# Optimization experiments

Measured on AMD Instinct MI355X. Metric: run time of the kernel, lower is better.

Reference implementation:

```python
import jax, jax.numpy as jnp
import numpy as np

D = 256      # hidden_size
H = 4        # num_attention_heads
DH = D // H  # dim per head = 64
L = 4        # num_hidden_layers
M = 266      # nb_features = int(64 * ln(64))
S = 4096     # seq len / max_position_embeddings
B = 4
LN_EPS = 1e-12


def layer_norm(x, g, b, eps=LN_EPS):
    mu = jnp.mean(x, -1, keepdims=True)
    var = jnp.var(x, -1, keepdims=True)
    return (x - mu) / jnp.sqrt(var + eps) * g + b


def softmax_kernel(x, proj, is_query, eps=1e-4):
    # x: [b,h,s,d], proj: [m,d] -> phi(x): [b,h,s,m] (FAVOR+ positive features)
    d = x.shape[-1]
    m = proj.shape[0]
    dn = d ** -0.25
    ratio = m ** -0.5
    dash = jnp.einsum('bhsd,md->bhsm', x, proj) * dn
    diag = jnp.sum(x * x, -1, keepdims=True) * 0.5 * (dn * dn)
    if is_query:
        stab = jnp.max(dash, -1, keepdims=True)  # per-query stabilizer
    else:
        stab = jnp.max(dash)  # global stabilizer for keys
    return ratio * (jnp.exp(dash - diag - stab) + eps)


def favor_attention(x, proj, Wq, bq, Wk, bk, Wv, bv, Wo, bo):
    b, s, d = x.shape
    split = lambda t: t.reshape(b, s, H, DH).transpose(0, 2, 1, 3)  # [b,h,s,dh]
    q = split(x @ Wq + bq)
    k = split(x @ Wk + bk)
    v = split(x @ Wv + bv)
    qp = softmax_kernel(q, proj, True)   # [b,h,s,m]
    kp = softmax_kernel(k, proj, False)  # [b,h,s,m]
    ksum = kp.sum(axis=2)                                  # [b,h,m]
    d_inv = 1.0 / jnp.einsum('bhsm,bhm->bhs', qp, ksum)    # normalizer
    ctx = jnp.einsum('bhsm,bhse->bhme', kp, v)             # [b,h,m,dh]
    out = jnp.einsum('bhsm,bhme,bhs->bhse', qp, ctx, d_inv)
    out = out.transpose(0, 2, 1, 3).reshape(b, s, d)
    return out @ Wo + bo


def _forward(input_embs, attention_mask, pos_emb, ln_g, ln_b, proj,
             Wq, bq, Wk, bk, Wv, bv, Wo, bo, ln1_g, ln1_b,
             W1, b1, W2, b2, ln2_g, ln2_b, p1_w, p1_b, p2_w, p2_b):
    b, s, d = input_embs.shape
    x = input_embs + pos_emb[:s][None]
    x = layer_norm(x, ln_g, ln_b)  # dropout is identity at eval
    for i in range(L):
        x = x + favor_attention(layer_norm(x, ln1_g[i], ln1_b[i]), proj[i],
                                Wq[i], bq[i], Wk[i], bk[i], Wv[i], bv[i], Wo[i], bo[i])
        h = layer_norm(x, ln2_g[i], ln2_b[i])
        x = x + (jax.nn.gelu(h @ W1[i] + b1[i]) @ W2[i] + b2[i])
    # AttentionPooling
    e = jnp.tanh(x @ p1_w + p1_b)
    alpha = jnp.exp(e @ p2_w + p2_b)            # [b,s,1]
    alpha = alpha * attention_mask[..., None]
    alpha = alpha / (jnp.sum(alpha, 1, keepdims=True) + 1e-8)
    return jnp.einsum('bsd,bs->bd', x, alpha[..., 0])


def setup_inputs() -> dict:
    key = jax.random.key(0)
    ks = iter(jax.random.split(key, 32))
    std = 0.02
    nrm = lambda shape: jax.random.normal(next(ks), shape, jnp.float32)
    return {
        'input_embs': nrm((B, S, D)),
        'attention_mask': jnp.ones((B, S), jnp.float32),
        'pos_emb': nrm((S, D)) * std,
        'ln_g': jnp.ones((D,), jnp.float32), 'ln_b': jnp.zeros((D,), jnp.float32),
        'proj': nrm((L, M, DH)),
        'Wq': nrm((L, D, D)) * std, 'bq': jnp.zeros((L, D), jnp.float32),
        'Wk': nrm((L, D, D)) * std, 'bk': jnp.zeros((L, D), jnp.float32),
        'Wv': nrm((L, D, D)) * std, 'bv': jnp.zeros((L, D), jnp.float32),
        'Wo': nrm((L, D, D)) * std, 'bo': jnp.zeros((L, D), jnp.float32),
        'ln1_g': jnp.ones((L, D), jnp.float32), 'ln1_b': jnp.zeros((L, D), jnp.float32),
        'W1': nrm((L, D, 4 * D)) * std, 'b1': jnp.zeros((L, 4 * D), jnp.float32),
        'W2': nrm((L, 4 * D, D)) * std, 'b2': jnp.zeros((L, D), jnp.float32),
        'ln2_g': jnp.ones((L, D), jnp.float32), 'ln2_b': jnp.zeros((L, D), jnp.float32),
        'p1_w': nrm((D, D)) * std, 'p1_b': jnp.zeros((D,), jnp.float32),
        'p2_w': nrm((D, 1)) * std, 'p2_b': jnp.zeros((1,), jnp.float32),
    }


def reference(input_embs, attention_mask, pos_emb, ln_g, ln_b, proj,
              Wq, bq, Wk, bk, Wv, bv, Wo, bo, ln1_g, ln1_b,
              W1, b1, W2, b2, ln2_g, ln2_b, p1_w, p1_b, p2_w, p2_b):
    return _forward(input_embs, attention_mask, pos_emb, ln_g, ln_b, proj,
                    Wq, bq, Wk, bk, Wv, bv, Wo, bo, ln1_g, ln1_b,
                    W1, b1, W2, b2, ln2_g, ln2_b, p1_w, p1_b, p2_w, p2_b)
```

## Files before the change

### kernel.cpp

```cpp
#include <hip/hip_runtime.h>
#include <math.h>


#define WS_ALIGN(x) (((x) + 255) & ~(size_t)255)

#define DN 0.35355339059327373f
#define DIAGC 0.0625f
#define RATIO 0.06131393394849658f
#define FEPS 1e-4f

typedef __attribute__((__ext_vector_type__(8))) __bf16 bf16x8;
typedef __attribute__((__ext_vector_type__(4))) float f32x4;

__device__ __forceinline__ float wredsum(float v) {
    v += __shfl_xor(v, 32); v += __shfl_xor(v, 16); v += __shfl_xor(v, 8);
    v += __shfl_xor(v, 4);  v += __shfl_xor(v, 2);  v += __shfl_xor(v, 1);
    return v;
}
__device__ __forceinline__ float wredmax(float v) {
    v = fmaxf(v, __shfl_xor(v, 32)); v = fmaxf(v, __shfl_xor(v, 16));
    v = fmaxf(v, __shfl_xor(v, 8));  v = fmaxf(v, __shfl_xor(v, 4));
    v = fmaxf(v, __shfl_xor(v, 2));  v = fmaxf(v, __shfl_xor(v, 1));
    return v;
}

__device__ __forceinline__ unsigned short f2bf(float f) {
    unsigned u = __builtin_bit_cast(unsigned, f);
    return (unsigned short)((u + 0x7fffu + ((u >> 16) & 1u)) >> 16);
}
__device__ __forceinline__ float blo(unsigned x) { return __builtin_bit_cast(float, x << 16); }
__device__ __forceinline__ float bhi(unsigned x) { return __builtin_bit_cast(float, x & 0xffff0000u); }
__device__ __forceinline__ float sumsq8(uint4 u) {
    float s = 0.f;
    s += blo(u.x)*blo(u.x) + bhi(u.x)*bhi(u.x);
    s += blo(u.y)*blo(u.y) + bhi(u.y)*bhi(u.y);
    s += blo(u.z)*blo(u.z) + bhi(u.z)*bhi(u.z);
    s += blo(u.w)*blo(u.w) + bhi(u.w)*bhi(u.w);
    return s;
}
__device__ __forceinline__ unsigned pack2(float a, float b) {
    return (unsigned)f2bf(a) | ((unsigned)f2bf(b) << 16);
}

__device__ __forceinline__ void gload_lds16(const unsigned short* g, unsigned short* lds) {
    __builtin_amdgcn_global_load_lds(
        (const __attribute__((address_space(1))) unsigned int*)g,
        (__attribute__((address_space(3))) unsigned int*)lds, 16, 0, 0);
}

__global__ __launch_bounds__(256) void add_ln2_kernel(
    const float* __restrict__ in, const float* __restrict__ pos,
    const float* __restrict__ g0, const float* __restrict__ b0,
    const float* __restrict__ g1, const float* __restrict__ b1,
    float* __restrict__ xout, unsigned short* __restrict__ hout)
{
    int row = blockIdx.x, t = threadIdx.x;
    __shared__ float sred[4];
    float v = in[(size_t)row * 256 + t] + pos[(size_t)(row & 4095) * 256 + t];
    float s = wredsum(v);
    if ((t & 63) == 0) sred[t >> 6] = s;
    __syncthreads();
    float mean = (sred[0] + sred[1] + sred[2] + sred[3]) * (1.0f / 256.0f);
    float d = v - mean;
    __syncthreads();
    float sq = wredsum(d * d);
    if ((t & 63) == 0) sred[t >> 6] = sq;
    __syncthreads();
    float var = (sred[0] + sred[1] + sred[2] + sred[3]) * (1.0f / 256.0f);
    float y1 = d * rsqrtf(var + 1e-12f) * g0[t] + b0[t];
    xout[(size_t)row * 256 + t] = y1;
    __syncthreads();
    float s1 = wredsum(y1);
    if ((t & 63) == 0) sred[t >> 6] = s1;
    __syncthreads();
    float mean1 = (sred[0] + sred[1] + sred[2] + sred[3]) * (1.0f / 256.0f);
    float d1 = y1 - mean1;
    __syncthreads();
    float sq1 = wredsum(d1 * d1);
    if ((t & 63) == 0) sred[t >> 6] = sq1;
    __syncthreads();
    float var1 = (sred[0] + sred[1] + sred[2] + sred[3]) * (1.0f / 256.0f);
    hout[(size_t)row * 256 + t] = f2bf(d1 * rsqrtf(var1 + 1e-12f) * g1[t] + b1[t]);
}

__global__ __launch_bounds__(256) void cast_transpose_kernel(
    const float* __restrict__ in, unsigned short* __restrict__ out, int R, int C)
{
    __shared__ float tile[32][33];
    size_t zo = (size_t)blockIdx.z * R * C;
    int c0 = blockIdx.x * 32, r0 = blockIdx.y * 32;
    int t = threadIdx.x, tc = t & 31, tr = t >> 5;
#pragma unroll
    for (int j = 0; j < 4; j++)
        tile[tr + j * 8][tc] = in[zo + (size_t)(r0 + tr + j * 8) * C + c0 + tc];
    __syncthreads();
#pragma unroll
    for (int j = 0; j < 4; j++) {
        int cc = tr + j * 8, rr = tc;
        out[zo + (size_t)(c0 + cc) * R + r0 + rr] = f2bf(tile[rr][cc]);
    }
}

__global__ __launch_bounds__(256) void cast_transpose4_kernel(
    const float* __restrict__ i0, const float* __restrict__ i1,
    const float* __restrict__ i2, const float* __restrict__ i3,
    unsigned short* __restrict__ o0, unsigned short* __restrict__ o1,
    unsigned short* __restrict__ o2, unsigned short* __restrict__ o3)
{
    __shared__ float tile[32][33];
    int z = blockIdx.z;
    int which = z >> 2, layer = z & 3;
    const float* in = (which == 0) ? i0 : (which == 1) ? i1 : (which == 2) ? i2 : i3;
    unsigned short* out = (which == 0) ? o0 : (which == 1) ? o1 : (which == 2) ? o2 : o3;
    size_t zo = (size_t)layer * 65536;
    int c0 = blockIdx.x * 32, r0 = blockIdx.y * 32;
    int t = threadIdx.x, tc = t & 31, tr = t >> 5;
#pragma unroll
    for (int j = 0; j < 4; j++)
        tile[tr + j * 8][tc] = in[zo + (size_t)(r0 + tr + j * 8) * 256 + c0 + tc];
    __syncthreads();
#pragma unroll
    for (int j = 0; j < 4; j++) {
        int cc = tr + j * 8, rr = tc;
        out[zo + (size_t)(c0 + cc) * 256 + r0 + rr] = f2bf(tile[rr][cc]);
    }
}

__global__ __launch_bounds__(256) void proj_cast_kernel(
    const float* __restrict__ proj, unsigned short* __restrict__ projbf)
{
    int idx = blockIdx.x * 256 + threadIdx.x;
    if (idx >= 10240) return;
    int li = idx / 2560; int rem = idx - li * 2560;
    int m = rem >> 3; int c = rem & 7;
    uint4 pk = {0, 0, 0, 0};
    if (m < 266) {
        const float* src = proj + ((size_t)li * 266 + m) * 64 + c * 8;
        float4 f0 = *(const float4*)(src);
        float4 f1 = *(const float4*)(src + 4);
        pk.x = pack2(f0.x, f0.y); pk.y = pack2(f0.z, f0.w);
        pk.z = pack2(f1.x, f1.y); pk.w = pack2(f1.z, f1.w);
    }
    *(uint4*)(projbf + (size_t)idx * 8) = pk;
}

__global__ __launch_bounds__(256) void ctx_cast_kernel(
    const float* __restrict__ ctxT, unsigned short* __restrict__ ctxbf)
{
    int idx = blockIdx.x * 256 + threadIdx.x;
    int row = idx / 36;
    int c = idx - row * 36;
    int m = c * 8;
    uint4 pk = {0, 0, 0, 0};
    if (m < 272) {
        const float* src = ctxT + (size_t)row * 272 + m;
        float4 f0 = *(const float4*)(src);
        float4 f1 = *(const float4*)(src + 4);
        pk.x = pack2(f0.x, f0.y); pk.y = pack2(f0.z, f0.w);
        pk.z = pack2(f1.x, f1.y); pk.w = pack2(f1.z, f1.w);
    }
    *(uint4*)(ctxbf + (size_t)row * 288 + c * 8) = pk;
}

__global__ __launch_bounds__(256) void qkv_kernel(
    const unsigned short* __restrict__ A,
    const unsigned short* __restrict__ Wqt, const unsigned short* __restrict__ Wkt,
    const unsigned short* __restrict__ Wvt,
    const float* __restrict__ bq, const float* __restrict__ bk, const float* __restrict__ bv,
    unsigned short* __restrict__ qbf, unsigned short* __restrict__ kbf,
    unsigned short* __restrict__ vT)
{
    __shared__ unsigned short As[2][4096];
    __shared__ unsigned short Bs[2][2048];
    const int K = 256;
    int t = threadIdx.x;
    int bm = blockIdx.y * 128, bn = blockIdx.x * 64;
    int grp = bn >> 8, lbn = bn & 255;
    const unsigned short* Bt = (grp == 0) ? Wqt : (grp == 1) ? Wkt : Wvt;
    const float* bias = (grp == 0) ? bq : (grp == 1) ? bk : bv;
    int w = t >> 6, l = t & 63, lm16 = l & 15, quad = l >> 4;
    int gc8 = ((l & 3) ^ ((l >> 3) & 3)) * 8;
    int rc8 = (quad ^ ((lm16 >> 1) & 3)) * 8;
    const unsigned short* pa0 = A + (size_t)(bm + w * 16 + (l >> 2)) * K + gc8;
    const unsigned short* pa1 = pa0 + (size_t)64 * K;
    const unsigned short* pb0 = Bt + (size_t)(lbn + w * 16 + (l >> 2)) * K + gc8;
    auto stage = [&](int buf, int k0) {
        gload_lds16(pa0 + k0, &As[buf][w * 512]);
        gload_lds16(pa1 + k0, &As[buf][w * 512 + 2048]);
        gload_lds16(pb0 + k0, &Bs[buf][w * 512]);
    };
    stage(0, 0);
    f32x4 acc[2][4] = {};
    __syncthreads();
    for (int kt = 0; kt < 8; ++kt) {
        int cur = kt & 1;
        if (kt < 7) stage(cur ^ 1, (kt + 1) * 32);
        bf16x8 af[2], bfr[4];
        af[0] = *(const bf16x8*)&As[cur][(w * 32 + lm16) * 32 + rc8];
        af[1] = *(const bf16x8*)&As[cur][(w * 32 + 16 + lm16) * 32 + rc8];
#pragma unroll
        for (int j = 0; j < 4; j++) bfr[j] = *(const bf16x8*)&Bs[cur][(j * 16 + lm16) * 32 + rc8];
#pragma unroll
        for (int i = 0; i < 2; i++)
#pragma unroll
            for (int j = 0; j < 4; j++)
                acc[i][j] = __builtin_amdgcn_mfma_f32_16x16x32_bf16(af[i], bfr[j], acc[i][j], 0, 0, 0);
        __syncthreads();
    }
#pragma unroll
    for (int i = 0; i < 2; i++)
#pragma unroll
        for (int j = 0; j < 4; j++) {
            int lcol = lbn + j * 16 + lm16;
            float bs = bias[lcol];
            int h = lcol >> 6, e = lcol & 63;
#pragma unroll
            for (int r = 0; r < 4; r++) {
                int row = bm + w * 32 + i * 16 + quad * 4 + r;
                int b = row >> 12, s = row & 4095;
                float v = acc[i][j][r] + bs;
                if (grp == 0)
                    qbf[((size_t)((b << 2) + h) * 4096 + s) * 64 + e] = f2bf(v);
                else if (grp == 1)
                    kbf[((size_t)((b << 2) + h) * 4096 + s) * 64 + e] = f2bf(v);
                else
                    vT[((size_t)((b << 2) + h) * 64 + e) * 4096 + s] = f2bf(v);
            }
        }
}

__global__ __launch_bounds__(256) void ffn1_kernel(
    const unsigned short* __restrict__ A, const unsigned short* __restrict__ Bt,
    const float* __restrict__ bias, unsigned short* __restrict__ Cb, int N, int K)
{
    __shared__ unsigned short As[2][4096];
    __shared__ unsigned short Bs[2][2048];
    int t = threadIdx.x;
    int bm = blockIdx.y * 128, bn = blockIdx.x * 64;
    int w = t >> 6, l = t & 63, lm16 = l & 15, quad = l >> 4;
    int gc8 = ((l & 3) ^ ((l >> 3) & 3)) * 8;
    int rc8 = (quad ^ ((lm16 >> 1) & 3)) * 8;
    const unsigned short* pa0 = A + (size_t)(bm + w * 16 + (l >> 2)) * K + gc8;
    const unsigned short* pa1 = pa0 + (size_t)64 * K;
    const unsigned short* pb0 = Bt + (size_t)(bn + w * 16 + (l >> 2)) * K + gc8;
    auto stage = [&](int buf, int k0) {
        gload_lds16(pa0 + k0, &As[buf][w * 512]);
        gload_lds16(pa1 + k0, &As[buf][w * 512 + 2048]);
        gload_lds16(pb0 + k0, &Bs[buf][w * 512]);
    };
    stage(0, 0);
    f32x4 acc[2][4] = {};
    __syncthreads();
    int nt = K >> 5;
    for (int kt = 0; kt < nt; ++kt) {
        int cur = kt & 1;
        if (kt < nt - 1) stage(cur ^ 1, (kt + 1) * 32);
        bf16x8 af[2], bfr[4];
        af[0] = *(const bf16x8*)&As[cur][(w * 32 + lm16) * 32 + rc8];
        af[1] = *(const bf16x8*)&As[cur][(w * 32 + 16 + lm16) * 32 + rc8];
#pragma unroll
        for (int j = 0; j < 4; j++) bfr[j] = *(const bf16x8*)&Bs[cur][(j * 16 + lm16) * 32 + rc8];
#pragma unroll
        for (int i = 0; i < 2; i++)
#pragma unroll
            for (int j = 0; j < 4; j++)
                acc[i][j] = __builtin_amdgcn_mfma_f32_16x16x32_bf16(af[i], bfr[j], acc[i][j], 0, 0, 0);
        __syncthreads();
    }
#pragma unroll
    for (int i = 0; i < 2; i++)
#pragma unroll
        for (int j = 0; j < 4; j++) {
            int col = bn + j * 16 + lm16;
            float bsv = bias[col];
#pragma unroll
            for (int r = 0; r < 4; r++) {
                int row = bm + w * 32 + i * 16 + quad * 4 + r;
                float v = acc[i][j][r] + bsv;
                float inner = 0.7978845608028654f * (v + 0.044715f * v * v * v);
                float gl = 0.5f * v * (1.0f + tanhf(inner));
                Cb[(size_t)row * N + col] = f2bf(gl);
            }
        }
}

template <int EPI>
__global__ __launch_bounds__(512) void gemm_fullrow_kernel(
    const unsigned short* __restrict__ A, const unsigned short* __restrict__ Bt,
    const float* __restrict__ bias, float* __restrict__ xio,
    const float* __restrict__ lng, const float* __restrict__ lnb,
    unsigned short* __restrict__ outb,
    const float* __restrict__ p2w, const float* __restrict__ p2b,
    const float* __restrict__ mask, float* __restrict__ alphab, int K)
{
    __shared__ unsigned short As2[2][2048];
    __shared__ unsigned short Bs2[2][8192];
    float (*red)[64] = (float (*)[64])As2;
    int t = threadIdx.x;
    int bm = blockIdx.x * 64;
    int w = t >> 6, l = t & 63, lm16 = l & 15, quad = l >> 4;
    int gc8 = ((l & 3) ^ ((l >> 3) & 3)) * 8;
    int rc8 = (quad ^ ((lm16 >> 1) & 3)) * 8;
    const unsigned short* pa = A + (size_t)(bm + (w & 3) * 16 + (l >> 2)) * K + gc8;
    const unsigned short* pb0 = Bt + (size_t)(w * 16 + (l >> 2)) * K + gc8;
    const unsigned short* pb1 = pb0 + (size_t)128 * K;
    auto stage = [&](int buf, int k0) {
        if (w < 4) gload_lds16(pa + k0, &As2[buf][w * 512]);
        gload_lds16(pb0 + k0, &Bs2[buf][w * 512]);
        gload_lds16(pb1 + k0, &Bs2[buf][w * 512 + 4096]);
    };
    stage(0, 0);
    f32x4 acc[4][2] = {};
    __syncthreads();
    int nt = K >> 5;
    for (int kt = 0; kt < nt; ++kt) {
        int cur = kt & 1;
        if (kt < nt - 1) stage(cur ^ 1, (kt + 1) * 32);
        bf16x8 af[4], bfv[2];
#pragma unroll
        for (int i = 0; i < 4; i++) af[i] = *(const bf16x8*)&As2[cur][(i * 16 + lm16) * 32 + rc8];
#pragma unroll
        for (int j = 0; j < 2; j++) bfv[j] = *(const bf16x8*)&Bs2[cur][(w * 32 + j * 16 + lm16) * 32 + rc8];
#pragma unroll
        for (int i = 0; i < 4; i++)
#pragma unroll
            for (int j = 0; j < 2; j++)
                acc[i][j] = __builtin_amdgcn_mfma_f32_16x16x32_bf16(af[i], bfv[j], acc[i][j], 0, 0, 0);
        __syncthreads();
    }
    int colbase = w * 32;
    if (EPI == 2) {
        float rs[4][4] = {};
#pragma unroll
        for (int j = 0; j < 2; j++) {
            int col = colbase + j * 16 + lm16;
            float bs = bias[col], pw = p2w[col];
#pragma unroll
            for (int i = 0; i < 4; i++)
#pragma unroll
                for (int r = 0; r < 4; r++)
                    rs[i][r] += tanhf(acc[i][j][r] + bs) * pw;
        }
#pragma unroll
        for (int m2 = 1; m2 <= 8; m2 <<= 1)
#pragma unroll
            for (int i = 0; i < 4; i++)
#pragma unroll
                for (int r = 0; r < 4; r++) rs[i][r] += __shfl_xor(rs[i][r], m2);
        __syncthreads();
        if (lm16 == 0) {
#pragma unroll
            for (int i = 0; i < 4; i++)
#pragma unroll
                for (int r = 0; r < 4; r++) red[w][i * 16 + quad * 4 + r] = rs[i][r];
        }
        __syncthreads();
        if (t < 64) {
            float sc = p2b[0];
#pragma unroll
            for (int ww = 0; ww < 8; ww++) sc += red[ww][t];
            int row = bm + t;
            alphab[row] = expf(sc) * mask[row];
        }
        return;
    }
    float rs[4][4] = {};
#pragma unroll
    for (int j = 0; j < 2; j++) {
        int col = colbase + j * 16 + lm16;
        float bs = bias[col];
#pragma unroll
        for (int i = 0; i < 4; i++)
#pragma unroll
            for (int r = 0; r < 4; r++) {
                int row = bm + i * 16 + quad * 4 + r;
                float v = acc[i][j][r] + bs + xio[(size_t)row * 256 + col];
                acc[i][j][r] = v;
                rs[i][r] += v;
            }
    }
    float mean[4][4], rstd[4][4];
    if (EPI == 0) {
#pragma unroll
        for (int m2 = 1; m2 <= 8; m2 <<= 1)
#pragma unroll
            for (int i = 0; i < 4; i++)
#pragma unroll
                for (int r = 0; r < 4; r++) rs[i][r] += __shfl_xor(rs[i][r], m2);
        __syncthreads();
        if (lm16 == 0) {
#pragma unroll
            for (int i = 0; i < 4; i++)
#pragma unroll
                for (int r = 0; r < 4; r++) red[w][i * 16 + quad * 4 + r] = rs[i][r];
        }
        __syncthreads();
        float vs[4][4] = {};
#pragma unroll
        for (int i = 0; i < 4; i++)
#pragma unroll
            for (int r = 0; r < 4; r++) {
                int rr = i * 16 + quad * 4 + r;
                float s = 0.f;
#pragma unroll
                for (int ww = 0; ww < 8; ww++) s += red[ww][rr];
                mean[i][r] = s * (1.0f / 256.0f);
            }
#pragma unroll
        for (int j = 0; j < 2; j++)
#pragma unroll
            for (int i = 0; i < 4; i++)
#pragma unroll
                for (int r = 0; r < 4; r++) {
                    float d = acc[i][j][r] - mean[i][r];
                    vs[i][r] += d * d;
                }
#pragma unroll
        for (int m2 = 1; m2 <= 8; m2 <<= 1)
#pragma unroll
            for (int i = 0; i < 4; i++)
#pragma unroll
                for (int r = 0; r < 4; r++) vs[i][r] += __shfl_xor(vs[i][r], m2);
        __syncthreads();
        if (lm16 == 0) {
#pragma unroll
            for (int i = 0; i < 4; i++)
#pragma unroll
                for (int r = 0; r < 4; r++) red[w][i * 16 + quad * 4 + r] = vs[i][r];
        }
        __syncthreads();
#pragma unroll
        for (int i = 0; i < 4; i++)
#pragma unroll
            for (int r = 0; r < 4; r++) {
                int rr = i * 16 + quad * 4 + r;
                float s = 0.f;
#pragma unroll
                for (int ww = 0; ww < 8; ww++) s += red[ww][rr];
                rstd[i][r] = rsqrtf(s * (1.0f / 256.0f) + 1e-12f);
            }
    }
#pragma unroll
    for (int j = 0; j < 2; j++) {
        int col = colbase + j * 16 + lm16;
        float g  = (EPI == 0) ? lng[col] : 0.f;
        float bb = (EPI == 0) ? lnb[col] : 0.f;
#pragma unroll
        for (int i = 0; i < 4; i++)
#pragma unroll
            for (int r = 0; r < 4; r++) {
                int row = bm + i * 16 + quad * 4 + r;
                float v = acc[i][j][r];
                xio[(size_t)row * 256 + col] = v;
                float y = (EPI == 0) ? ((v - mean[i][r]) * rstd[i][r] * g + bb) : v;
                outb[(size_t)row * 256 + col] = f2bf(y);
            }
    }
}

#define ZERO_FLOATS 282880
__global__ __launch_bounds__(256) void phi_kmax_kernel(
    const unsigned short* __restrict__ kbf, const unsigned short* __restrict__ projbf,
    float* __restrict__ pmax, float* __restrict__ zbase)
{
    __shared__ uint4 As[64][9];
    __shared__ uint4 Bs[272][8];
    __shared__ float diag_s[64];
    __shared__ float sred[4];
    int t = threadIdx.x;
    int s0 = blockIdx.x * 64;
    int bh = blockIdx.y;
    int w = t >> 6, l = t & 63, lm16 = l & 15, quad = l >> 4;
    {
        int bid = blockIdx.y * 64 + blockIdx.x;
        for (int i = bid * 256 + t; i < ZERO_FLOATS; i += 1024 * 256) zbase[i] = 0.f;
    }
    {
        int arow = t >> 2, akoff = (t & 3) * 16;
        const uint4* ga = (const uint4*)(kbf + ((size_t)bh * 4096 + s0 + arow) * 64 + akoff);
        uint4 u0 = ga[0], u1 = ga[1];
        As[arow][(akoff >> 3)] = u0; As[arow][(akoff >> 3) + 1] = u1;
        float ss = sumsq8(u0) + sumsq8(u1);
        ss += __shfl_xor(ss, 1); ss += __shfl_xor(ss, 2);
        if ((t & 3) == 0) diag_s[arow] = DIAGC * ss;
    }
    {
        unsigned short* Pl = (unsigned short*)Bs;
        int gcp8 = ((l & 7) ^ ((l >> 3) & 7)) * 8;
        const unsigned short* ps = projbf + (size_t)(l >> 3) * 64 + gcp8;
        for (int i = w; i < 34; i += 4)
            gload_lds16(ps + (size_t)i * 512, Pl + i * 512);
    }
    __syncthreads();
    f32x4 acc[17] = {};
#pragma unroll
    for (int ks = 0; ks < 2; ks++) {
        bf16x8 af = *(const bf16x8*)&As[w * 16 + lm16][ks * 4 + quad];
#pragma unroll
        for (int j = 0; j < 17; j++) {
            bf16x8 bfv = *(const bf16x8*)&Bs[j * 16 + lm16][(ks * 4 + quad) ^ (lm16 & 7)];
            acc[j] = __builtin_amdgcn_mfma_f32_16x16x32_bf16(af, bfv, acc[j], 0, 0, 0);
        }
    }
    int rloc = w * 16 + quad * 4;
    float kmax = -1e30f;
#pragma unroll
    for (int j = 0; j < 17; j++) {
        int m = j * 16 + lm16;
        bool valid = m < 266;
#pragma unroll
        for (int r = 0; r < 4; r++)
            if (valid) kmax = fmaxf(kmax, acc[j][r] * DN - diag_s[rloc + r]);
    }
    kmax = wredmax(kmax);
    if (l == 0) sred[w] = kmax;
    __syncthreads();
    if (t == 0)
        pmax[(size_t)bh * 64 + blockIdx.x] =
            fmaxf(fmaxf(sred[0], sred[1]), fmaxf(sred[2], sred[3]));
}

__global__ __launch_bounds__(256) void ctx_fused_kernel(
    const unsigned short* __restrict__ kbf, const unsigned short* __restrict__ vT,
    const unsigned short* __restrict__ projbf, const float* __restrict__ pmax,
    float* __restrict__ ksum, float* __restrict__ ctxT)
{
    __shared__ uint4 Ap[64][8];
    __shared__ uint4 Ks[64][9];
    __shared__ uint4 Vs[64][9];
    __shared__ unsigned short kp_s[64][72];
    __shared__ float diag_s[64];
    __shared__ float sred2[4];
    int t = threadIdx.x;
    int m0 = blockIdx.x * 64;
    int bh = blockIdx.y;
    int sb = blockIdx.z * 512;
    int w = t >> 6, l = t & 63, lm16 = l & 15, quad = l >> 4;
    {
        unsigned short* Pl = (unsigned short*)Ap;
        int gcp8 = ((l & 7) ^ ((l >> 3) & 7)) * 8;
        const unsigned short* ps = projbf + (size_t)(m0 + (l >> 3)) * 64 + gcp8;
        for (int i = w; i < 8; i += 4)
            gload_lds16(ps + (size_t)i * 512, Pl + i * 512);
    }
    float pm = -1e30f;
    for (int i = t; i < 1024; i += 256) pm = fmaxf(pm, pmax[i]);
    pm = wredmax(pm);
    if (l == 0) sred2[w] = pm;
    __syncthreads();
    float st = fmaxf(fmaxf(sred2[0], sred2[1]), fmaxf(sred2[2], sred2[3]));
    f32x4 accc[4] = {};
    float ksacc[4] = {0.f, 0.f, 0.f, 0.f};
    int srow = t >> 2, skoff = (t & 3) * 16;
    for (int kc = 0; kc < 8; kc++) {
        int sc = sb + kc * 64;
        const uint4* gk = (const uint4*)(kbf + ((size_t)bh * 4096 + sc + srow) * 64 + skoff);
        uint4 k0 = gk[0], k1 = gk[1];
        const uint4* gv = (const uint4*)(vT + ((size_t)bh * 64 + srow) * 4096 + sc + skoff);
        uint4 v0 = gv[0], v1 = gv[1];
        __syncthreads();
        Ks[srow][(skoff >> 3)] = k0; Ks[srow][(skoff >> 3) + 1] = k1;
        Vs[srow][(skoff >> 3)] = v0; Vs[srow][(skoff >> 3) + 1] = v1;
        float ss = sumsq8(k0) + sumsq8(k1);
        ss += __shfl_xor(ss, 1); ss += __shfl_xor(ss, 2);
        if ((t & 3) == 0) diag_s[srow] = DIAGC * ss;
        __syncthreads();
        f32x4 accd[4] = {};
#pragma unroll
        for (int ks = 0; ks < 2; ks++) {
            bf16x8 af = *(const bf16x8*)&Ap[w * 16 + lm16][(ks * 4 + quad) ^ (lm16 & 7)];
#pragma unroll
            for (int j = 0; j < 4; j++) {
                bf16x8 bfv = *(const bf16x8*)&Ks[j * 16 + lm16][ks * 4 + quad];
                accd[j] = __builtin_amdgcn_mfma_f32_16x16x32_bf16(af, bfv, accd[j], 0, 0, 0);
            }
        }
        int mbase = m0 + w * 16 + quad * 4;
#pragma unroll
        for (int j = 0; j < 4; j++) {
            int s_loc = j * 16 + lm16;
            float dgv = diag_s[s_loc];
#pragma unroll
            for (int r = 0; r < 4; r++) {
                float v = accd[j][r] * DN - dgv;
                float e = (mbase + r < 266) ? RATIO * (__expf(v - st) + FEPS) : 0.f;
                kp_s[w * 16 + quad * 4 + r][s_loc] = f2bf(e);
                ksacc[r] += e;
            }
        }
        __syncthreads();
#pragma unroll
        for (int ks = 0; ks < 2; ks++) {
            bf16x8 af = *(const bf16x8*)&Vs[w * 16 + lm16][ks * 4 + quad];
#pragma unroll
            for (int jt = 0; jt < 4; jt++) {
                bf16x8 bfv = *(const bf16x8*)&kp_s[jt * 16 + lm16][ks * 32 + quad * 8];
                accc[jt] = __builtin_amdgcn_mfma_f32_16x16x32_bf16(af, bfv, accc[jt], 0, 0, 0);
            }
        }
    }
#pragma unroll
    for (int r = 0; r < 4; r++) {
        float v = ksacc[r];
        v += __shfl_xor(v, 1); v += __shfl_xor(v, 2);
        v += __shfl_xor(v, 4); v += __shfl_xor(v, 8);
        if (lm16 == 0) {
            int m = m0 + w * 16 + quad * 4 + r;
            if (m < 272) atomicAdd(&ksum[bh * 272 + m], v);
        }
    }
#pragma unroll
    for (int jt = 0; jt < 4; jt++) {
        int m = m0 + jt * 16 + lm16;
        if (m >= 272) continue;
#pragma unroll
        for (int r = 0; r < 4; r++) {
            int e = w * 16 + quad * 4 + r;
            atomicAdd(&ctxT[((size_t)bh * 64 + e) * 272 + m], accc[jt][r]);
        }
    }
}

__global__ __launch_bounds__(256) void phi_q_attn_kernel(
    const unsigned short* __restrict__ qbf, const unsigned short* __restrict__ projbf,
    const float* __restrict__ ksum, const unsigned short* __restrict__ ctxbf,
    unsigned short* __restrict__ abf)
{
    __shared__ uint4 uA[1152];
    __shared__ uint4 bufB[272][8];
    __shared__ float diag_s[64];
    __shared__ float den_s[64];
    int t = threadIdx.x;
    int s0 = blockIdx.x * 64;
    int bh = blockIdx.y;
    int w = t >> 6, l = t & 63, lm16 = l & 15, quad = l >> 4;
    uint4 (*bufA)[9] = (uint4(*)[9])uA;
    {
        int arow = t >> 2, akoff = (t & 3) * 16;
        const uint4* ga = (const uint4*)(qbf + ((size_t)bh * 4096 + s0 + arow) * 64 + akoff);
        uint4 u0 = ga[0], u1 = ga[1];
        bufA[arow][(akoff >> 3)] = u0; bufA[arow][(akoff >> 3) + 1] = u1;
        float ss = sumsq8(u0) + sumsq8(u1);
        ss += __shfl_xor(ss, 1); ss += __shfl_xor(ss, 2);
        if ((t & 3) == 0) diag_s[arow] = DIAGC * ss;
    }
    {
        unsigned short* Pl = (unsigned short*)bufB;
        int gcp8 = ((l & 7) ^ ((l >> 3) & 7)) * 8;
        const unsigned short* ps = projbf + (size_t)(l >> 3) * 64 + gcp8;
        for (int i = w; i < 34; i += 4)
            gload_lds16(ps + (size_t)i * 512, Pl + i * 512);
    }
    float ksv[17];
#pragma unroll
    for (int j = 0; j < 17; j++) ksv[j] = ksum[bh * 272 + j * 16 + lm16];
    __syncthreads();
    f32x4 acc[17] = {};
#pragma unroll
    for (int ks = 0; ks < 2; ks++) {
        bf16x8 af = *(const bf16x8*)&bufA[w * 16 + lm16][ks * 4 + quad];
#pragma unroll
        for (int j = 0; j < 17; j++) {
            bf16x8 bfv = *(const bf16x8*)&bufB[j * 16 + lm16][(ks * 4 + quad) ^ (lm16 & 7)];
            acc[j] = __builtin_amdgcn_mfma_f32_16x16x32_bf16(af, bfv, acc[j], 0, 0, 0);
        }
    }
    int rloc = w * 16 + quad * 4;
    float dg[4];
#pragma unroll
    for (int r = 0; r < 4; r++) dg[r] = diag_s[rloc + r];
    float vmax[4] = {-1e30f, -1e30f, -1e30f, -1e30f};
#pragma unroll
    for (int j = 0; j < 17; j++) {
        int m = j * 16 + lm16;
        bool valid = m < 266;
#pragma unroll
        for (int r = 0; r < 4; r++) {
            float v = acc[j][r] * DN - dg[r];
            acc[j][r] = v;
            if (valid) vmax[r] = fmaxf(vmax[r], v);
        }
    }
#pragma unroll
    for (int m2 = 1; m2 <= 8; m2 <<= 1)
#pragma unroll
        for (int r = 0; r < 4; r++) vmax[r] = fmaxf(vmax[r], __shfl_xor(vmax[r], m2));
    __syncthreads();
    unsigned short* ctxs = (unsigned short*)uA;
    const unsigned short* ctxg = ctxbf + (size_t)bh * 64 * 288;
    for (int i = w; i < 18; i += 4)
        gload_lds16(ctxg + i * 512 + l * 8, ctxs + i * 512);
    unsigned short* qp_s = (unsigned short*)bufB;
    float den[4] = {0.f, 0.f, 0.f, 0.f};
#pragma unroll
    for (int j = 0; j < 17; j++) {
        int m = j * 16 + lm16;
        bool valid = m < 266;
#pragma unroll
        for (int r = 0; r < 4; r++) {
            float e = valid ? RATIO * (__expf(acc[j][r] - vmax[r]) + FEPS) : 0.f;
            qp_s[(rloc + r) * 272 + m] = f2bf(e);
            den[r] += e * ksv[j];
        }
    }
#pragma unroll
    for (int m2 = 1; m2 <= 8; m2 <<= 1)
#pragma unroll
        for (int r = 0; r < 4; r++) den[r] += __shfl_xor(den[r], m2);
    if (lm16 == 0) {
#pragma unroll
        for (int r = 0; r < 4; r++) den_s[rloc + r] = den[r];
    }
    bf16x8 paf[9];
#pragma unroll
    for (int kk = 0; kk < 9; kk++)
        paf[kk] = *(const bf16x8*)&qp_s[(w * 16 + lm16) * 272 + kk * 32 + quad * 8];
    __syncthreads();
    int b = bh >> 2, h = bh & 3;
    f32x4 oacc[4] = {};
#pragma unroll
    for (int qd = 0; qd < 4; qd++) {
        const unsigned short* cs = ctxs + (qd & 1) * 4608;
#pragma unroll
        for (int kk = 0; kk < 9; kk++) {
            bf16x8 bfv = *(const bf16x8*)&cs[lm16 * 288 + kk * 32 + quad * 8];
            oacc[qd] = __builtin_amdgcn_mfma_f32_16x16x32_bf16(paf[kk], bfv, oacc[qd], 0, 0, 0);
        }
        if (qd < 3) {
            __syncthreads();
            if (qd < 2) {
                for (int i = w; i < 9; i += 4)
                    gload_lds16(ctxg + (qd + 2) * 4608 + i * 512 + l * 8,
                                ctxs + (qd & 1) * 4608 + i * 512);
            }
        }
    }
#pragma unroll
    for (int qd = 0; qd < 4; qd++) {
        int e = qd * 16 + lm16;
#pragma unroll
        for (int r = 0; r < 4; r++) {
            int sl = rloc + r;
            abf[((size_t)(b * 4096 + s0 + sl)) * 256 + h * 64 + e] = f2bf(oacc[qd][r] / den_s[sl]);
        }
    }
}

__global__ __launch_bounds__(256) void pool_denom_kernel(
    const float* __restrict__ alpha, float* __restrict__ denomb)
{
    __shared__ float sred[4];
    int b = blockIdx.x, t = threadIdx.x;
    float p = 0.f;
    for (int s = t; s < 4096; s += 256) p += alpha[b * 4096 + s];
    p = wredsum(p);
    if ((t & 63) == 0) sred[t >> 6] = p;
    __syncthreads();
    if (t == 0) denomb[b] = sred[0] + sred[1] + sred[2] + sred[3] + 1e-8f;
}

__global__ __launch_bounds__(256) void pool_out_kernel(
    const float* __restrict__ x, const float* __restrict__ alpha,
    const float* __restrict__ denomb, float* __restrict__ out)
{
    int b = blockIdx.x, chunk = blockIdx.y, t = threadIdx.x;
    float inv = 1.0f / denomb[b];
    float acc = 0.f;
    int s0 = chunk * 128;
    for (int s = s0; s < s0 + 128; s++)
        acc += x[((size_t)(b << 12) + s) * 256 + t] * alpha[(b << 12) + s];
    atomicAdd(&out[b * 256 + t], acc * inv);
}

extern "C" void kernel_launch(void* const* d_in, const int* in_sizes, int n_in,
                              void* d_out, int out_size, void* d_ws, size_t ws_size,
                              hipStream_t stream)
{
    const float* input_embs = (const float*)d_in[0];
    const float* mask  = (const float*)d_in[1];
    const float* pos   = (const float*)d_in[2];
    const float* ln_g  = (const float*)d_in[3];
    const float* ln_b  = (const float*)d_in[4];
    const float* proj  = (const float*)d_in[5];
    const float* Wq = (const float*)d_in[6];  const float* bq = (const float*)d_in[7];
    const float* Wk = (const float*)d_in[8];  const float* bk = (const float*)d_in[9];
    const float* Wv = (const float*)d_in[10]; const float* bv = (const float*)d_in[11];
    const float* Wo = (const float*)d_in[12]; const float* bo = (const float*)d_in[13];
    const float* ln1g = (const float*)d_in[14]; const float* ln1b = (const float*)d_in[15];
    const float* W1 = (const float*)d_in[16]; const float* b1 = (const float*)d_in[17];
    const float* W2 = (const float*)d_in[18]; const float* b2 = (const float*)d_in[19];
    const float* ln2g = (const float*)d_in[20]; const float* ln2b = (const float*)d_in[21];
    const float* p1w = (const float*)d_in[22]; const float* p1b = (const float*)d_in[23];
    const float* p2w = (const float*)d_in[24]; const float* p2b = (const float*)d_in[25];
    float* out = (float*)d_out;
    char* ws = (char*)d_ws;

    size_t off = 0;
    auto alloc = [&](size_t bytes) { size_t o = off; off += WS_ALIGN(bytes); return o; };
    float* xbuf = (float*)(ws + alloc(16384ull * 256 * 4));
    unsigned short* hbf = (unsigned short*)(ws + alloc(16384ull * 256 * 2));
    unsigned short* qbf = (unsigned short*)(ws + alloc(16384ull * 256 * 2));
    unsigned short* kbf = (unsigned short*)(ws + alloc(16384ull * 256 * 2));
    unsigned short* vT  = (unsigned short*)(ws + alloc(16384ull * 256 * 2));
    unsigned short* midbf = (unsigned short*)(ws + alloc(16384ull * 1024 * 2));
    size_t ksum_off = alloc(16ull * 272 * 4);
    float* ksum = (float*)(ws + ksum_off);
    float* ctxT = (float*)(ws + alloc(16ull * 64 * 272 * 4));
    float* pmaxb = (float*)(ws + alloc(1024ull * 4));
    float* alphab = (float*)(ws + alloc(16384ull * 4));
    float* pdenom = (float*)(ws + alloc(256));
    unsigned short* Wqt = (unsigned short*)(ws + alloc(4ull * 65536 * 2));
    unsigned short* Wkt = (unsigned short*)(ws + alloc(4ull * 65536 * 2));
    unsigned short* Wvt = (unsigned short*)(ws + alloc(4ull * 65536 * 2));
    unsigned short* Wot = (unsigned short*)(ws + alloc(4ull * 65536 * 2));
    unsigned short* W1t = (unsigned short*)(ws + alloc(4ull * 262144 * 2));
    unsigned short* W2t = (unsigned short*)(ws + alloc(4ull * 262144 * 2));
    unsigned short* projbf = (unsigned short*)(ws + alloc(4ull * 20480 * 2));
    unsigned short* p1t = (unsigned short*)(ws + alloc(65536ull * 2));
    unsigned short* ctxbf = (unsigned short*)(ws + alloc(16ull * 64 * 288 * 2));
    unsigned short* abf = hbf;

    cast_transpose4_kernel<<<dim3(8, 8, 16), 256, 0, stream>>>(Wq, Wk, Wv, Wo, Wqt, Wkt, Wvt, Wot);
    cast_transpose_kernel<<<dim3(32, 8, 4), 256, 0, stream>>>(W1, W1t, 256, 1024);
    cast_transpose_kernel<<<dim3(8, 32, 4), 256, 0, stream>>>(W2, W2t, 1024, 256);
    cast_transpose_kernel<<<dim3(8, 8, 1), 256, 0, stream>>>(p1w, p1t, 256, 256);
    proj_cast_kernel<<<40, 256, 0, stream>>>(proj, projbf);

    add_ln2_kernel<<<16384, 256, 0, stream>>>(input_embs, pos, ln_g, ln_b, ln1g, ln1b, xbuf, hbf);

    for (int i = 0; i < 4; i++) {
        const unsigned short* pj = projbf + (size_t)i * 20480;
        qkv_kernel<<<dim3(12, 128), 256, 0, stream>>>(hbf,
            Wqt + (size_t)i * 65536, Wkt + (size_t)i * 65536, Wvt + (size_t)i * 65536,
            bq + i * 256, bk + i * 256, bv + i * 256, qbf, kbf, vT);
        phi_kmax_kernel<<<dim3(64, 16), 256, 0, stream>>>(kbf, pj, pmaxb, ksum);
        ctx_fused_kernel<<<dim3(5, 16, 8), 256, 0, stream>>>(kbf, vT, pj, pmaxb, ksum, ctxT);
        ctx_cast_kernel<<<144, 256, 0, stream>>>(ctxT, ctxbf);
        phi_q_attn_kernel<<<dim3(64, 16), 256, 0, stream>>>(qbf, pj, ksum, ctxbf, abf);
        gemm_fullrow_kernel<0><<<256, 512, 0, stream>>>(abf, Wot + (size_t)i * 65536,
            bo + i * 256, xbuf, ln2g + i * 256, ln2b + i * 256, hbf,
            nullptr, nullptr, nullptr, nullptr, 256);
        ffn1_kernel<<<dim3(16, 128), 256, 0, stream>>>(hbf, W1t + (size_t)i * 262144,
            b1 + i * 1024, midbf, 1024, 256);
        if (i < 3)
            gemm_fullrow_kernel<0><<<256, 512, 0, stream>>>(midbf, W2t + (size_t)i * 262144,
                b2 + i * 256, xbuf, ln1g + (i + 1) * 256, ln1b + (i + 1) * 256, hbf,
                nullptr, nullptr, nullptr, nullptr, 1024);
        else
            gemm_fullrow_kernel<1><<<256, 512, 0, stream>>>(midbf, W2t + (size_t)i * 262144,
                b2 + i * 256, xbuf, nullptr, nullptr, hbf,
                nullptr, nullptr, nullptr, nullptr, 1024);
    }

    gemm_fullrow_kernel<2><<<256, 512, 0, stream>>>(hbf, p1t, p1b, nullptr, nullptr, nullptr,
        nullptr, p2w, p2b, mask, alphab, 256);
    pool_denom_kernel<<<4, 256, 0, stream>>>(alphab, pdenom);
    hipMemsetAsync(d_out, 0, (size_t)out_size * sizeof(float), stream);
    pool_out_kernel<<<dim3(4, 32), 256, 0, stream>>>(xbuf, alphab, pdenom, out);
}
```

Baseline: 801.1 us.

## Retile ctx_fused kernel to 144 features per block with prefetched K/V

The ctx_fused kernel now covers 144 random features per block instead of 64, so the grid shrinks from 5 to 2 feature tiles. This removes the padded fifth tile and cuts how often K and V are re-read across feature tiles. The sequence split goes from 8 to 16 chunks of 256 positions to keep enough blocks. Each wave now owns 16 sequence rows across nine feature subtiles, and the next K/V chunk is loaded into registers during compute. In exchange, register and shared-memory use per block rises (nine accumulators, larger kp_s and Ap), which may lower occupancy, and more blocks issue atomic adds.

```diff
diff --git a/kernel.cpp b/kernel.cpp
--- a/kernel.cpp
+++ b/kernel.cpp
@@ -525,67 +525,69 @@
     const unsigned short* __restrict__ projbf, const float* __restrict__ pmax,
     float* __restrict__ ksum, float* __restrict__ ctxT)
 {
-    __shared__ uint4 Ap[64][8];
+    __shared__ uint4 Ap[144][8];
     __shared__ uint4 Ks[64][9];
     __shared__ uint4 Vs[64][9];
-    __shared__ unsigned short kp_s[64][72];
+    __shared__ unsigned short kp_s[144][72];
     __shared__ float diag_s[64];
     __shared__ float sred2[4];
     int t = threadIdx.x;
-    int m0 = blockIdx.x * 64;
+    int m0 = blockIdx.x * 144;
     int bh = blockIdx.y;
-    int sb = blockIdx.z * 512;
+    int sb = blockIdx.z * 256;
     int w = t >> 6, l = t & 63, lm16 = l & 15, quad = l >> 4;
     {
         unsigned short* Pl = (unsigned short*)Ap;
         int gcp8 = ((l & 7) ^ ((l >> 3) & 7)) * 8;
         const unsigned short* ps = projbf + (size_t)(m0 + (l >> 3)) * 64 + gcp8;
-        for (int i = w; i < 8; i += 4)
+        for (int i = w; i < 18; i += 4)
             gload_lds16(ps + (size_t)i * 512, Pl + i * 512);
     }
     float pm = -1e30f;
     for (int i = t; i < 1024; i += 256) pm = fmaxf(pm, pmax[i]);
     pm = wredmax(pm);
     if (l == 0) sred2[w] = pm;
+    int srow = t >> 2, skoff = (t & 3) * 16, sk4 = skoff >> 3;
+    const uint4* gk = (const uint4*)(kbf + ((size_t)bh * 4096 + sb + srow) * 64 + skoff);
+    uint4 k0 = gk[0], k1 = gk[1];
+    const uint4* gv = (const uint4*)(vT + ((size_t)bh * 64 + srow) * 4096 + sb + skoff);
+    uint4 v0 = gv[0], v1 = gv[1];
     __syncthreads();
     float st = fmaxf(fmaxf(sred2[0], sred2[1]), fmaxf(sred2[2], sred2[3]));
-    f32x4 accc[4] = {};
-    float ksacc[4] = {0.f, 0.f, 0.f, 0.f};
-    int srow = t >> 2, skoff = (t & 3) * 16;
-    for (int kc = 0; kc < 8; kc++) {
-        int sc = sb + kc * 64;
-        const uint4* gk = (const uint4*)(kbf + ((size_t)bh * 4096 + sc + srow) * 64 + skoff);
-        uint4 k0 = gk[0], k1 = gk[1];
-        const uint4* gv = (const uint4*)(vT + ((size_t)bh * 64 + srow) * 4096 + sc + skoff);
-        uint4 v0 = gv[0], v1 = gv[1];
-        __syncthreads();
-        Ks[srow][(skoff >> 3)] = k0; Ks[srow][(skoff >> 3) + 1] = k1;
-        Vs[srow][(skoff >> 3)] = v0; Vs[srow][(skoff >> 3) + 1] = v1;
+    f32x4 accc[9] = {};
+    float ksacc[9][4] = {};
+    for (int kc = 0; kc < 4; kc++) {
+        if (kc) __syncthreads();
+        Ks[srow][sk4] = k0; Ks[srow][sk4 + 1] = k1;
+        Vs[srow][sk4] = v0; Vs[srow][sk4 + 1] = v1;
         float ss = sumsq8(k0) + sumsq8(k1);
         ss += __shfl_xor(ss, 1); ss += __shfl_xor(ss, 2);
         if ((t & 3) == 0) diag_s[srow] = DIAGC * ss;
         __syncthreads();
-        f32x4 accd[4] = {};
-#pragma unroll
-        for (int ks = 0; ks < 2; ks++) {
-            bf16x8 af = *(const bf16x8*)&Ap[w * 16 + lm16][(ks * 4 + quad) ^ (lm16 & 7)];
-#pragma unroll
-            for (int j = 0; j < 4; j++) {
-                bf16x8 bfv = *(const bf16x8*)&Ks[j * 16 + lm16][ks * 4 + quad];
-                accd[j] = __builtin_amdgcn_mfma_f32_16x16x32_bf16(af, bfv, accd[j], 0, 0, 0);
-            }
-        }
-        int mbase = m0 + w * 16 + quad * 4;
-#pragma unroll
-        for (int j = 0; j < 4; j++) {
-            int s_loc = j * 16 + lm16;
-            float dgv = diag_s[s_loc];
+        if (kc < 3) {
+            int sc = sb + (kc + 1) * 64;
+            const uint4* gk2 = (const uint4*)(kbf + ((size_t)bh * 4096 + sc + srow) * 64 + skoff);
+            k0 = gk2[0]; k1 = gk2[1];
+            const uint4* gv2 = (const uint4*)(vT + ((size_t)bh * 64 + srow) * 4096 + sc + skoff);
+            v0 = gv2[0]; v1 = gv2[1];
+        }
+        float dgv = diag_s[w * 16 + lm16];
+#pragma unroll
+        for (int jm = 0; jm < 9; jm++) {
+            f32x4 accd = {};
+#pragma unroll
+            for (int ks = 0; ks < 2; ks++) {
+                bf16x8 af = *(const bf16x8*)&Ap[jm * 16 + lm16][(ks * 4 + quad) ^ (lm16 & 7)];
+                bf16x8 bfv = *(const bf16x8*)&Ks[w * 16 + lm16][ks * 4 + quad];
+                accd = __builtin_amdgcn_mfma_f32_16x16x32_bf16(af, bfv, accd, 0, 0, 0);
+            }
 #pragma unroll
             for (int r = 0; r < 4; r++) {
-                float v = accd[j][r] * DN - dgv;
-                float e = (mbase + r < 266) ? RATIO * (__expf(v - st) + FEPS) : 0.f;
-                kp_s[w * 16 + quad * 4 + r][s_loc] = f2bf(e);
-                ksacc[r] += e;
+                int mg = m0 + jm * 16 + quad * 4 + r;
+                float v = accd[r] * DN - dgv;
+                float e = (mg < 266) ? RATIO * (__expf(v - st) + FEPS) : 0.f;
+                kp_s[jm * 16 + quad * 4 + r][w * 16 + lm16] = f2bf(e);
+                ksacc[jm][r] += e;
             }
         }
         __syncthreads();
@@ -593,30 +595,32 @@
         for (int ks = 0; ks < 2; ks++) {
             bf16x8 af = *(const bf16x8*)&Vs[w * 16 + lm16][ks * 4 + quad];
 #pragma unroll
-            for (int jt = 0; jt < 4; jt++) {
+            for (int jt = 0; jt < 9; jt++) {
                 bf16x8 bfv = *(const bf16x8*)&kp_s[jt * 16 + lm16][ks * 32 + quad * 8];
                 accc[jt] = __builtin_amdgcn_mfma_f32_16x16x32_bf16(af, bfv, accc[jt], 0, 0, 0);
             }
         }
     }
 #pragma unroll
-    for (int r = 0; r < 4; r++) {
-        float v = ksacc[r];
-        v += __shfl_xor(v, 1); v += __shfl_xor(v, 2);
-        v += __shfl_xor(v, 4); v += __shfl_xor(v, 8);
-        if (lm16 == 0) {
-            int m = m0 + w * 16 + quad * 4 + r;
-            if (m < 272) atomicAdd(&ksum[bh * 272 + m], v);
-        }
-    }
-#pragma unroll
-    for (int jt = 0; jt < 4; jt++) {
-        int m = m0 + jt * 16 + lm16;
-        if (m >= 272) continue;
+    for (int jm = 0; jm < 9; jm++)
+#pragma unroll
+        for (int r = 0; r < 4; r++) {
+            float vv = ksacc[jm][r];
+            vv += __shfl_xor(vv, 1); vv += __shfl_xor(vv, 2);
+            vv += __shfl_xor(vv, 4); vv += __shfl_xor(vv, 8);
+            if (lm16 == 0) {
+                int mg = m0 + jm * 16 + quad * 4 + r;
+                if (mg < 272) atomicAdd(&ksum[bh * 272 + mg], vv);
+            }
+        }
+#pragma unroll
+    for (int jt = 0; jt < 9; jt++) {
+        int mg = m0 + jt * 16 + lm16;
+        if (mg >= 272) continue;
 #pragma unroll
         for (int r = 0; r < 4; r++) {
             int e = w * 16 + quad * 4 + r;
-            atomicAdd(&ctxT[((size_t)bh * 64 + e) * 272 + m], accc[jt][r]);
+            atomicAdd(&ctxT[((size_t)bh * 64 + e) * 272 + mg], accc[jt][r]);
         }
     }
 }
@@ -834,7 +838,7 @@
             Wqt + (size_t)i * 65536, Wkt + (size_t)i * 65536, Wvt + (size_t)i * 65536,
             bq + i * 256, bk + i * 256, bv + i * 256, qbf, kbf, vT);
         phi_kmax_kernel<<<dim3(64, 16), 256, 0, stream>>>(kbf, pj, pmaxb, ksum);
-        ctx_fused_kernel<<<dim3(5, 16, 8), 256, 0, stream>>>(kbf, vT, pj, pmaxb, ksum, ctxT);
+        ctx_fused_kernel<<<dim3(2, 16, 16), 256, 0, stream>>>(kbf, vT, pj, pmaxb, ksum, ctxT);
         ctx_cast_kernel<<<144, 256, 0, stream>>>(ctxT, ctxbf);
         phi_q_attn_kernel<<<dim3(64, 16), 256, 0, stream>>>(qbf, pj, ksum, ctxbf, abf);
         gemm_fullrow_kernel<0><<<256, 512, 0, stream>>>(abf, Wot + (size_t)i * 65536,
```

Result: slower. 844.6 us (+5.4%).
